# Performance work log

Measured on AMD Instinct MI355X. Metric: run time of the kernel, lower is better.

The kernel has to match this reference:

```python
import jax, jax.numpy as jnp
import numpy as np

N_NODES = 20000
N_EDGES = 320000
MUL = 64            # multiplicity of 0e and 1o in hidden/out irreps
NUM_BASIS = 8
INV_SQRT3 = 0.5773502691896258
EPS = 1e-5


def setup_inputs() -> dict:
    key = jax.random.key(0)
    k = jax.random.split(key, 16)
    return {
        "node_hiddens": jax.random.normal(k[0], (N_NODES, 4 * MUL), dtype=jnp.float32),
        "edge_attr": jax.random.uniform(k[1], (N_EDGES, NUM_BASIS), dtype=jnp.float32),
        "edge_sh": jax.random.normal(k[2], (N_EDGES, 4), dtype=jnp.float32),
        "w1_s": jax.random.normal(k[3], (MUL, MUL), dtype=jnp.float32),
        "w1_v": jax.random.normal(k[4], (MUL, MUL), dtype=jnp.float32),
        "wsc_s": jax.random.normal(k[5], (MUL, MUL), dtype=jnp.float32),
        "wsc_v": jax.random.normal(k[6], (MUL, MUL), dtype=jnp.float32),
        "w2_s": jax.random.normal(k[7], (2 * MUL, MUL), dtype=jnp.float32),
        "w2_v": jax.random.normal(k[8], (2 * MUL, MUL), dtype=jnp.float32),
        "fc_w1": jax.random.normal(k[9], (NUM_BASIS, 64), dtype=jnp.float32),
        "fc_w2": jax.random.normal(k[10], (64, 64), dtype=jnp.float32),
        "fc_w3": jax.random.normal(k[11], (64, 4 * MUL), dtype=jnp.float32),
        "g_s": jnp.ones((MUL,), dtype=jnp.float32),
        "g_v": jnp.ones((MUL,), dtype=jnp.float32),
        "edge_index": jax.random.randint(k[12], (2, N_EDGES), 0, N_NODES),
    }


def reference(node_hiddens, edge_attr, edge_sh, w1_s, w1_v, wsc_s, wsc_v,
              w2_s, w2_v, fc_w1, fc_w2, fc_w3, g_s, g_v, edge_index):
    N = node_hiddens.shape[0]
    # e3nn layout: [N, 64x0e | 64x1o] with mul-major vectors
    xs = node_hiddens[:, :MUL]                        # [N, 64]
    xv = node_hiddens[:, MUL:].reshape(N, MUL, 3)     # [N, 64, 3]

    # edge MLP (FullyConnectedNet([8,64,64,256], silu)) -> per-edge TP weights
    h = jax.nn.silu(edge_attr @ fc_w1 * (1.0 / np.sqrt(float(NUM_BASIS))))
    h = jax.nn.silu(h @ fc_w2 * (1.0 / np.sqrt(64.0)))
    w = h @ fc_w3 * (1.0 / np.sqrt(64.0))             # [E, 4*MUL]
    wA, wB, wC, wD = jnp.split(w, 4, axis=1)          # one 64-vec per uvu path

    inv = 1.0 / np.sqrt(float(MUL))
    # self-connection Linear(hidden -> out)
    sc_s = xs @ wsc_s * inv
    sc_v = jnp.einsum('nud,uv->nvd', xv, wsc_v) * inv
    # linear_1 Linear(hidden -> hidden)
    ys = xs @ w1_s * inv
    yv = jnp.einsum('nud,uv->nvd', xv, w1_v) * inv

    src = edge_index[0]
    dst = edge_index[1]
    es = ys[dst]                                      # [E, 64] gather
    ev = yv[dst]                                      # [E, 64, 3]
    sh0 = edge_sh[:, :1]                              # [E, 1]
    sh1 = edge_sh[:, 1:]                              # [E, 3]

    # weighted uvu Clebsch-Gordan tensor product -> irreps_mid (sorted order)
    m0a = wA * es * sh0                                          # 0e x 0e -> 0e
    m0b = wD * jnp.einsum('eud,ed->eu', ev, sh1) * INV_SQRT3     # 1o x 1o -> 0e
    m1a = wB[:, :, None] * es[:, :, None] * sh1[:, None, :]      # 0e x 1o -> 1o
    m1b = wC[:, :, None] * ev * sh0[:, :, None]                  # 1o x 0e -> 1o
    mid_s = jnp.concatenate([m0a, m0b], axis=1)       # [E, 128]
    mid_v = jnp.concatenate([m1a, m1b], axis=1)       # [E, 128, 3]

    # scatter-sum to source nodes + 1/sqrt(degree) normalization
    ns = jax.ops.segment_sum(mid_s, src, num_segments=N)
    nv = jax.ops.segment_sum(mid_v, src, num_segments=N)
    deg = jax.ops.segment_sum(jnp.ones((src.shape[0],), node_hiddens.dtype), src, num_segments=N)
    dn = jax.lax.rsqrt(jnp.maximum(deg, 1.0))
    ns = ns * dn[:, None]
    nv = nv * dn[:, None, None]

    # linear_2 Linear(128x0e+128x1o -> 64x0e+64x1o) + self connection
    inv2 = 1.0 / np.sqrt(2.0 * MUL)
    os_ = ns @ w2_s * inv2 + sc_s
    ov = jnp.einsum('nud,uv->nvd', nv, w2_v) * inv2 + sc_v

    # equivariant RMS layer norm per irrep type (centering=False)
    os_ = os_ * jax.lax.rsqrt(jnp.mean(os_ * os_, axis=1, keepdims=True) + EPS) * g_s
    rms_v = jax.lax.rsqrt(jnp.mean(ov * ov, axis=(1, 2))[:, None, None] + EPS)
    ov = ov * rms_v * g_v[None, :, None]

    return jnp.concatenate([os_, ov.reshape(N, 3 * MUL)], axis=1)
```

## Files before the change

### kernel.cpp

```cpp
#include <hip/hip_runtime.h>
#include <math.h>

#define N_NODES 20000
#define N_EDGES 320000
#define N_TILES 1250
#define PACK_BLOCKS 32
#define HIST_BLOCKS ((N_EDGES + 255) / 256)
#define SCAT_BLOCKS ((N_EDGES + 255) / 256)
#define K1_BLOCKS ((N_TILES + 3) / 4)

typedef __attribute__((ext_vector_type(8))) short bf16x8;
typedef __attribute__((ext_vector_type(4))) float f32x4;
typedef __attribute__((ext_vector_type(2))) unsigned u32x2;
typedef __attribute__((ext_vector_type(4))) unsigned u32x4;

__device__ __forceinline__ float silu_f(float x) {
    return x / (1.0f + __expf(-x));
}
__device__ __forceinline__ short f2bf(float x) {
    union { float f; unsigned u; } v; v.f = x;
    unsigned r = (v.u + 0x7FFFu + ((v.u >> 16) & 1u)) >> 16;
    return (short)r;
}
__device__ __forceinline__ float blo(unsigned u) { return __uint_as_float(u << 16); }
__device__ __forceinline__ float bhi(unsigned u) { return __uint_as_float(u & 0xFFFF0000u); }
__device__ __forceinline__ unsigned cvt_pk(float lo, float hi) {
    unsigned r;
    asm("v_cvt_pk_bf16_f32 %0, %1, %2" : "=v"(r) : "v"(lo), "v"(hi));
    return r;
}
#define MFMA16(a, b, c) __builtin_amdgcn_mfma_f32_16x16x32_bf16((a), (b), (c), 0, 0, 0)

__global__ __launch_bounds__(256) void kp_hist(
    const int* __restrict__ eidx, int* __restrict__ cnt,
    const float* __restrict__ fcw1, const float* __restrict__ fcw2,
    const float* __restrict__ fcw3,
    const float* __restrict__ w1s, const float* __restrict__ wscs,
    const float* __restrict__ w1v, const float* __restrict__ wscv,
    const float* __restrict__ w2s, const float* __restrict__ w2v,
    short* __restrict__ w1A, short* __restrict__ w2A, short* __restrict__ w3A,
    short* __restrict__ wp1, short* __restrict__ wp2)
{
    if (blockIdx.x >= PACK_BLOCKS) {
        const int e = (blockIdx.x - PACK_BLOCKS) * 256 + threadIdx.x;
        if (e < N_EDGES) atomicAdd(&cnt[eidx[e]], 1);
        return;
    }
    const int tid = blockIdx.x * 256 + threadIdx.x;
    const int nthr = PACK_BLOCKS * 256;
    for (int i = tid; i < 4*64*8; i += nthr) {
        const int j = i & 7, lane = (i >> 3) & 63, t = i >> 9;
        const int k = (lane >> 4) * 8 + j, row = t*16 + (lane & 15);
        w1A[i] = (k < 8) ? f2bf(fcw1[k*64 + row]) : (short)0;
    }
    for (int i = tid; i < 8*64*8; i += nthr) {
        const int j = i & 7, lane = (i >> 3) & 63, kk = (i >> 9) & 1, t = i >> 10;
        const int k = kk*32 + (lane >> 4)*8 + j, row = t*16 + (lane & 15);
        w2A[i] = f2bf(fcw2[k*64 + row]);
    }
    for (int i = tid; i < 32*64*8; i += nthr) {
        const int j = i & 7, lane = (i >> 3) & 63, kk = (i >> 9) & 1, Tp = i >> 10;
        const int c = Tp >> 2, q = Tp & 3;
        const int k = kk*32 + (lane >> 4)*8 + j;
        const int ch = (q*4 + c)*16 + (lane & 15);
        const float s = (ch >= 192) ? 0.5773502691896258f : 1.0f;
        w3A[i] = f2bf(fcw3[(size_t)k*256 + ch] * s);
    }
    for (int i = tid; i < 4096; i += nthr) {
        const int j = i & 7, lane = (i >> 3) & 63, kk = (i >> 9) & 1, vt = i >> 10;
        const int row = vt*16 + (lane & 15), k = kk*32 + (lane >> 4)*8 + j;
        wp1[i]         = f2bf(w1s [k*64 + row]);
        wp1[4096 + i]  = f2bf(wscs[k*64 + row]);
        wp1[8192 + i]  = f2bf(w1v [k*64 + row]);
        wp1[12288 + i] = f2bf(wscv[k*64 + row]);
    }
    for (int i = tid; i < 8192; i += nthr) {
        const int j = i & 7, lane = (i >> 3) & 63, kk = (i >> 9) & 3, vt = i >> 11;
        const int row = vt*16 + (lane & 15), k = kk*32 + (lane >> 4)*8 + j;
        const int r = (k & 1)*64 + (k >> 1);
        wp2[i]        = f2bf(w2s[r*64 + row]);
        wp2[8192 + i] = f2bf(w2v[r*64 + row]);
    }
}

__global__ __launch_bounds__(1024) void s_scan(int* __restrict__ cnt,
                                               int* __restrict__ start) {
    const int tid = threadIdx.x;
    const int base = tid * 20;
    int vals[20];
    int sum = 0;
    #pragma unroll
    for (int j = 0; j < 20; ++j) {
        const int i = base + j;
        const int v = (i < N_NODES) ? cnt[i] : 0;
        vals[j] = sum;
        sum += v;
    }
    const int lane = tid & 63, wv = tid >> 6;
    int x = sum;
    #pragma unroll
    for (int off = 1; off < 64; off <<= 1) {
        const int t = __shfl_up(x, off);
        if (lane >= off) x += t;
    }
    __shared__ int wtot[16];
    if (lane == 63) wtot[wv] = x;
    __syncthreads();
    int wpref = 0;
    for (int k = 0; k < wv; ++k) wpref += wtot[k];
    const int excl = wpref + x - sum;
    #pragma unroll
    for (int j = 0; j < 20; ++j) {
        const int i = base + j;
        if (i < N_NODES) {
            const int s = excl + vals[j];
            start[i] = s;
            cnt[i] = s;
        }
    }
    if (tid == 1023) start[N_NODES] = wpref + x;
}

__global__ __launch_bounds__(256) void scat_k1(
    const int* __restrict__ eidx, int* __restrict__ cursor,
    int* __restrict__ perm, int* __restrict__ dst_perm,
    const float* __restrict__ nh, const short* __restrict__ wp1,
    short* __restrict__ ydata, short* __restrict__ scpack)
{
    if (blockIdx.x < SCAT_BLOCKS) {
        const int e = blockIdx.x * 256 + threadIdx.x;
        if (e < N_EDGES) {
            const int src = eidx[e];
            const int pos = atomicAdd(&cursor[src], 1);
            perm[pos] = e;
            dst_perm[pos] = eidx[N_EDGES + e];
        }
        return;
    }
    const int lane = threadIdx.x & 63;
    const int tile = (blockIdx.x - SCAT_BLOCKS) * 4 + (threadIdx.x >> 6);
    if (tile >= N_TILES) return;
    const int l15 = lane & 15, lhi = lane >> 4;
    const int n = tile*16 + l15;
    const float* row = nh + (size_t)n * 256;
    const f32x4 zz = {0.f, 0.f, 0.f, 0.f};
    f32x4 acc[8][4];
    #pragma unroll
    for (int c = 0; c < 8; ++c)
        #pragma unroll
        for (int vt = 0; vt < 4; ++vt) acc[c][vt] = zz;

    #pragma unroll
    for (int kk = 0; kk < 2; ++kk) {
        const int k0 = kk*32 + lhi*8;
        const float4 s0 = *(const float4*)(row + k0);
        const float4 s1 = *(const float4*)(row + k0 + 4);
        float4 vv[6];
        #pragma unroll
        for (int q = 0; q < 6; ++q) vv[q] = *(const float4*)(row + 64 + 3*k0 + q*4);
        const float* vf = (const float*)vv;
        union { u32x4 u; bf16x8 v; } bs, b0, b1, b2;
        bs.u[0] = cvt_pk(s0.x, s0.y); bs.u[1] = cvt_pk(s0.z, s0.w);
        bs.u[2] = cvt_pk(s1.x, s1.y); bs.u[3] = cvt_pk(s1.z, s1.w);
        #pragma unroll
        for (int q = 0; q < 4; ++q) {
            b0.u[q] = cvt_pk(vf[6*q + 0], vf[6*q + 3]);
            b1.u[q] = cvt_pk(vf[6*q + 1], vf[6*q + 4]);
            b2.u[q] = cvt_pk(vf[6*q + 2], vf[6*q + 5]);
        }
        #pragma unroll
        for (int vt = 0; vt < 4; ++vt) {
            const int fo = ((vt*2 + kk)*64 + lane)*8;
            const bf16x8 a_ys = *(const bf16x8*)&wp1[fo];
            const bf16x8 a_ss = *(const bf16x8*)&wp1[4096 + fo];
            const bf16x8 a_yv = *(const bf16x8*)&wp1[8192 + fo];
            const bf16x8 a_sv = *(const bf16x8*)&wp1[12288 + fo];
            acc[0][vt] = MFMA16(a_ys, bs.v, acc[0][vt]);
            acc[1][vt] = MFMA16(a_ss, bs.v, acc[1][vt]);
            acc[2][vt] = MFMA16(a_yv, b0.v, acc[2][vt]);
            acc[3][vt] = MFMA16(a_yv, b1.v, acc[3][vt]);
            acc[4][vt] = MFMA16(a_yv, b2.v, acc[4][vt]);
            acc[5][vt] = MFMA16(a_sv, b0.v, acc[5][vt]);
            acc[6][vt] = MFMA16(a_sv, b1.v, acc[6][vt]);
            acc[7][vt] = MFMA16(a_sv, b2.v, acc[7][vt]);
        }
    }
    #pragma unroll
    for (int vt = 0; vt < 4; ++vt)
        #pragma unroll
        for (int r = 0; r < 4; ++r) {
            const int v = vt*16 + lhi*4 + r;
            u32x2 yo, so;
            yo[0] = cvt_pk(acc[0][vt][r]*0.125f, acc[2][vt][r]*0.125f);
            yo[1] = cvt_pk(acc[3][vt][r]*0.125f, acc[4][vt][r]*0.125f);
            so[0] = cvt_pk(acc[1][vt][r]*0.125f, acc[5][vt][r]*0.125f);
            so[1] = cvt_pk(acc[6][vt][r]*0.125f, acc[7][vt][r]*0.125f);
            *(u32x2*)&ydata [((size_t)n*64 + v)*4] = yo;
            *(u32x2*)&scpack[((size_t)n*64 + v)*4] = so;
        }
}

__global__ __launch_bounds__(256) void k_mlp(
    const float* __restrict__ ea, const int* __restrict__ perm,
    const short* __restrict__ w1A, const short* __restrict__ w2A,
    const short* __restrict__ w3A, short* __restrict__ wq)
{
    __shared__ short hb1[4][1024];
    __shared__ short hb2[4][1024];
    const int lane = threadIdx.x & 63, w = threadIdx.x >> 6;
    const int l15 = lane & 15, lhi = lane >> 4;
    const int wbase = (blockIdx.x * 4 + w) * 32;
    short* h1b = hb1[w];
    short* h2b = hb2[w];
    const int swz = (l15 & 7) << 4;
    const f32x4 zz = {0.f, 0.f, 0.f, 0.f};

    bf16x8 a1[4], a2[4][2];
    #pragma unroll
    for (int t = 0; t < 4; ++t)
        a1[t] = *(const bf16x8*)&w1A[(t*64 + lane)*8];
    #pragma unroll
    for (int t = 0; t < 4; ++t)
        #pragma unroll
        for (int kk = 0; kk < 2; ++kk)
            a2[t][kk] = *(const bf16x8*)&w2A[((t*2 + kk)*64 + lane)*8];

    bf16x8 bh2[2][2];
    #pragma unroll
    for (int sb = 0; sb < 2; ++sb) {
        bf16x8 bea = {0,0,0,0,0,0,0,0};
        if (lhi == 0) {
            const int e = perm[wbase + sb*16 + l15];
            const float4 p0 = *(const float4*)(ea + (size_t)e*8);
            const float4 p1 = *(const float4*)(ea + (size_t)e*8 + 4);
            union { u32x4 u; bf16x8 v; } tu;
            tu.u[0] = cvt_pk(p0.x, p0.y);
            tu.u[1] = cvt_pk(p0.z, p0.w);
            tu.u[2] = cvt_pk(p1.x, p1.y);
            tu.u[3] = cvt_pk(p1.z, p1.w);
            bea = tu.v;
        }
        f32x4 d1[4];
        #pragma unroll
        for (int t = 0; t < 4; ++t)
            d1[t] = MFMA16(a1[t], bea, zz);
        #pragma unroll
        for (int t = 0; t < 4; ++t) {
            const float s0 = silu_f(d1[t][0] * 0.35355339059327373f);
            const float s1 = silu_f(d1[t][1] * 0.35355339059327373f);
            const float s2 = silu_f(d1[t][2] * 0.35355339059327373f);
            const float s3 = silu_f(d1[t][3] * 0.35355339059327373f);
            u32x2 pk; pk[0] = cvt_pk(s0, s1); pk[1] = cvt_pk(s2, s3);
            const int byt = (l15*128 + t*32 + lhi*8) ^ swz;
            *(u32x2*)((char*)h1b + byt) = pk;
        }
        bf16x8 bh1[2];
        #pragma unroll
        for (int kk = 0; kk < 2; ++kk)
            bh1[kk] = *(const bf16x8*)((const char*)h1b + ((l15*128 + kk*64 + lhi*16) ^ swz));
        f32x4 d2[4];
        #pragma unroll
        for (int t = 0; t < 4; ++t) {
            d2[t] = MFMA16(a2[t][0], bh1[0], zz);
            d2[t] = MFMA16(a2[t][1], bh1[1], d2[t]);
        }
        #pragma unroll
        for (int t = 0; t < 4; ++t) {
            const float s0 = silu_f(d2[t][0] * 0.125f) * 0.125f;
            const float s1 = silu_f(d2[t][1] * 0.125f) * 0.125f;
            const float s2 = silu_f(d2[t][2] * 0.125f) * 0.125f;
            const float s3 = silu_f(d2[t][3] * 0.125f) * 0.125f;
            u32x2 pk; pk[0] = cvt_pk(s0, s1); pk[1] = cvt_pk(s2, s3);
            const int byt = (l15*128 + t*32 + lhi*8) ^ swz;
            *(u32x2*)((char*)h2b + byt) = pk;
        }
        #pragma unroll
        for (int kk = 0; kk < 2; ++kk)
            bh2[sb][kk] = *(const bf16x8*)((const char*)h2b + ((l15*128 + kk*64 + lhi*16) ^ swz));
    }

    #pragma unroll
    for (int c = 0; c < 4; ++c) {
        f32x4 dq[4][2];
        #pragma unroll
        for (int q = 0; q < 4; ++q) {
            const int Tp = c*4 + q;
            const bf16x8 a30 = *(const bf16x8*)&w3A[((Tp*2 + 0)*64 + lane)*8];
            const bf16x8 a31 = *(const bf16x8*)&w3A[((Tp*2 + 1)*64 + lane)*8];
            #pragma unroll
            for (int sb = 0; sb < 2; ++sb) {
                f32x4 d = MFMA16(a30, bh2[sb][0], zz);
                dq[q][sb] = MFMA16(a31, bh2[sb][1], d);
            }
        }
        #pragma unroll
        for (int sb = 0; sb < 2; ++sb) {
            const int slot = wbase + sb*16 + l15;
            const int vbase = c*16 + lhi*4;
            u32x4 lo, hi;
            lo[0] = cvt_pk(dq[0][sb][0], dq[1][sb][0]);
            lo[1] = cvt_pk(dq[2][sb][0], dq[3][sb][0]);
            lo[2] = cvt_pk(dq[0][sb][1], dq[1][sb][1]);
            lo[3] = cvt_pk(dq[2][sb][1], dq[3][sb][1]);
            hi[0] = cvt_pk(dq[0][sb][2], dq[1][sb][2]);
            hi[1] = cvt_pk(dq[2][sb][2], dq[3][sb][2]);
            hi[2] = cvt_pk(dq[0][sb][3], dq[1][sb][3]);
            hi[3] = cvt_pk(dq[2][sb][3], dq[3][sb][3]);
            short* base = &wq[((size_t)slot*64 + vbase)*4];
            *(u32x4*)(base)     = lo;
            *(u32x4*)(base + 8) = hi;
        }
    }
}

__global__ __launch_bounds__(256) void k2_gather(
    const int* __restrict__ start, const int* __restrict__ perm,
    const int* __restrict__ dst_perm, const float* __restrict__ esh,
    const short* __restrict__ wq, const short* __restrict__ ydata,
    unsigned* __restrict__ ncat32)
{
    const int lane = threadIdx.x & 63;
    const int n = blockIdx.x * 4 + (threadIdx.x >> 6);
    if (n >= N_NODES) return;
    const int s0 = start[n], s1 = start[n + 1];
    float acc0=0.f, acc1=0.f, av0=0.f, av1=0.f, av2=0.f, bv0=0.f, bv1=0.f, bv2=0.f;
    for (int p = s0; p < s1; p += 8) {
        const int m = s1 - p;
        u32x2 wv[8], yd[8];
        float4 sh[8];
        int e[8], d[8];
        #pragma unroll
        for (int j = 0; j < 8; ++j) {
            const int pp = (j < m) ? p + j : s0;
            e[j] = perm[pp];
            d[j] = dst_perm[pp];
            wv[j] = *(const u32x2*)&wq[((size_t)pp*64 + lane)*4];
        }
        #pragma unroll
        for (int j = 0; j < 8; ++j) {
            sh[j] = *(const float4*)(esh + (size_t)e[j]*4);
            yd[j] = *(const u32x2*)&ydata[((size_t)d[j]*64 + lane)*4];
        }
        #pragma unroll
        for (int j = 0; j < 8; ++j) {
            const float g = (j < m) ? 1.f : 0.f;
            const float wa = blo(wv[j][0])*g, wb = bhi(wv[j][0])*g;
            const float wc = blo(wv[j][1])*g, wd = bhi(wv[j][1])*g;
            const float es  = blo(yd[j][0]), ev0 = bhi(yd[j][0]);
            const float ev1 = blo(yd[j][1]), ev2 = bhi(yd[j][1]);
            acc0 += wa * es * sh[j].x;
            acc1 += wd * (ev0*sh[j].y + ev1*sh[j].z + ev2*sh[j].w);
            const float esb = wb * es;
            av0 += esb * sh[j].y; av1 += esb * sh[j].z; av2 += esb * sh[j].w;
            const float c0 = wc * sh[j].x;
            bv0 += c0 * ev0; bv1 += c0 * ev1; bv2 += c0 * ev2;
        }
    }
    unsigned* nrow = ncat32 + (size_t)n * 256;
    nrow[lane]        = cvt_pk(acc0, acc1);
    nrow[64  + lane]  = cvt_pk(av0, bv0);
    nrow[128 + lane]  = cvt_pk(av1, bv1);
    nrow[192 + lane]  = cvt_pk(av2, bv2);
}

__global__ __launch_bounds__(256) void k3_mfma(
    const unsigned* __restrict__ ncat32, const int* __restrict__ start,
    const short* __restrict__ wp2, const short* __restrict__ scpack,
    const float* __restrict__ gs, const float* __restrict__ gv,
    float* __restrict__ out)
{
    const int lane = threadIdx.x & 63;
    const int tile = blockIdx.x * 4 + (threadIdx.x >> 6);
    if (tile >= N_TILES) return;
    const int l15 = lane & 15, lhi = lane >> 4;
    const int n = tile*16 + l15;
    const f32x4 zz = {0.f, 0.f, 0.f, 0.f};
    f32x4 acc[4][4];
    #pragma unroll
    for (int c = 0; c < 4; ++c)
        #pragma unroll
        for (int vt = 0; vt < 4; ++vt) acc[c][vt] = zz;

    const size_t nb = (size_t)n * 256;
    #pragma unroll
    for (int kk = 0; kk < 4; ++kk) {
        const int uo = kk*16 + lhi*4;
        union { u32x4 u; bf16x8 v; } bs, b0, b1, b2;
        bs.u = *(const u32x4*)&ncat32[nb +        uo];
        b0.u = *(const u32x4*)&ncat32[nb +  64 + uo];
        b1.u = *(const u32x4*)&ncat32[nb + 128 + uo];
        b2.u = *(const u32x4*)&ncat32[nb + 192 + uo];
        #pragma unroll
        for (int vt = 0; vt < 4; ++vt) {
            const int fo = ((vt*4 + kk)*64 + lane)*8;
            const bf16x8 a_s = *(const bf16x8*)&wp2[fo];
            const bf16x8 a_v = *(const bf16x8*)&wp2[8192 + fo];
            acc[0][vt] = MFMA16(a_s, bs.v, acc[0][vt]);
            acc[1][vt] = MFMA16(a_v, b0.v, acc[1][vt]);
            acc[2][vt] = MFMA16(a_v, b1.v, acc[2][vt]);
            acc[3][vt] = MFMA16(a_v, b2.v, acc[3][vt]);
        }
    }
    const float degf = (float)(start[n+1] - start[n]);
    const float coef = rsqrtf(fmaxf(degf, 1.0f)) * 0.08838834764831845f;
    float os[4][4], o0[4][4], o1[4][4], o2[4][4];
    float ssq = 0.f, vsq = 0.f;
    #pragma unroll
    for (int vt = 0; vt < 4; ++vt)
        #pragma unroll
        for (int r = 0; r < 4; ++r) {
            const int v = vt*16 + lhi*4 + r;
            const u32x2 sc = *(const u32x2*)&scpack[((size_t)n*64 + v)*4];
            os[vt][r] = acc[0][vt][r]*coef + blo(sc[0]);
            o0[vt][r] = acc[1][vt][r]*coef + bhi(sc[0]);
            o1[vt][r] = acc[2][vt][r]*coef + blo(sc[1]);
            o2[vt][r] = acc[3][vt][r]*coef + bhi(sc[1]);
            ssq += os[vt][r]*os[vt][r];
            vsq += o0[vt][r]*o0[vt][r] + o1[vt][r]*o1[vt][r] + o2[vt][r]*o2[vt][r];
        }
    ssq += __shfl_xor(ssq, 16); ssq += __shfl_xor(ssq, 32);
    vsq += __shfl_xor(vsq, 16); vsq += __shfl_xor(vsq, 32);
    const float rs = rsqrtf(ssq * (1.0f/64.0f) + 1e-5f);
    const float rv = rsqrtf(vsq * (1.0f/192.0f) + 1e-5f);
    float* orow = out + (size_t)n * 256;
    #pragma unroll
    for (int vt = 0; vt < 4; ++vt) {
        const int vb = vt*16 + lhi*4;
        const float4 g4  = *(const float4*)(gs + vb);
        const float4 gv4 = *(const float4*)(gv + vb);
        const float4 so = { os[vt][0]*rs*g4.x, os[vt][1]*rs*g4.y,
                            os[vt][2]*rs*g4.z, os[vt][3]*rs*g4.w };
        *(float4*)(orow + vb) = so;
        const float m0 = rv*gv4.x, m1 = rv*gv4.y, m2 = rv*gv4.z, m3 = rv*gv4.w;
        const float4 w0 = { o0[vt][0]*m0, o1[vt][0]*m0, o2[vt][0]*m0, o0[vt][1]*m1 };
        const float4 w1 = { o1[vt][1]*m1, o2[vt][1]*m1, o0[vt][2]*m2, o1[vt][2]*m2 };
        const float4 w2 = { o2[vt][2]*m2, o0[vt][3]*m3, o1[vt][3]*m3, o2[vt][3]*m3 };
        float* vbase = orow + 64 + vb*3;
        *(float4*)(vbase)     = w0;
        *(float4*)(vbase + 4) = w1;
        *(float4*)(vbase + 8) = w2;
    }
}

extern "C" void kernel_launch(void* const* d_in, const int* in_sizes, int n_in,
                              void* d_out, int out_size, void* d_ws, size_t ws_size,
                              hipStream_t stream) {
    const float* nh   = (const float*)d_in[0];
    const float* ea   = (const float*)d_in[1];
    const float* esh  = (const float*)d_in[2];
    const float* w1s  = (const float*)d_in[3];
    const float* w1v  = (const float*)d_in[4];
    const float* wscs = (const float*)d_in[5];
    const float* wscv = (const float*)d_in[6];
    const float* w2s  = (const float*)d_in[7];
    const float* w2v  = (const float*)d_in[8];
    const float* fcw1 = (const float*)d_in[9];
    const float* fcw2 = (const float*)d_in[10];
    const float* fcw3 = (const float*)d_in[11];
    const float* gs   = (const float*)d_in[12];
    const float* gv   = (const float*)d_in[13];
    const int*   eidx = (const int*)d_in[14];
    float* out = (float*)d_out;

    char* wsb = (char*)d_ws;
    size_t off = 0;
    short* ydata  = (short*)(wsb + off); off += (size_t)N_NODES * 256 * 2;
    short* scpack = (short*)(wsb + off); off += (size_t)N_NODES * 256 * 2;
    unsigned* ncat32 = (unsigned*)(wsb + off); off += (size_t)N_NODES * 256 * 4;
    int* cnt      = (int*)(wsb + off); off += (size_t)N_NODES * 4;
    int* start    = (int*)(wsb + off); off += ((size_t)N_NODES + 1) * 4;
    int* perm     = (int*)(wsb + off); off += (size_t)N_EDGES * 4;
    int* dst_perm = (int*)(wsb + off); off += (size_t)N_EDGES * 4;
    short* w1A = (short*)(wsb + off); off += 2048 * 2;
    short* w2A = (short*)(wsb + off); off += 4096 * 2;
    short* w3A = (short*)(wsb + off); off += 16384 * 2;
    short* wp1 = (short*)(wsb + off); off += 16384 * 2;
    short* wp2 = (short*)(wsb + off); off += 16384 * 2;
    off = (off + 15) & ~(size_t)15;
    short* wq = (short*)(wsb + off);

    hipMemsetAsync(cnt, 0, N_NODES * sizeof(int), stream);

    kp_hist<<<PACK_BLOCKS + HIST_BLOCKS, 256, 0, stream>>>(
        eidx, cnt, fcw1, fcw2, fcw3, w1s, wscs, w1v, wscv, w2s, w2v,
        w1A, w2A, w3A, wp1, wp2);

    s_scan<<<1, 1024, 0, stream>>>(cnt, start);

    scat_k1<<<SCAT_BLOCKS + K1_BLOCKS, 256, 0, stream>>>(
        eidx, cnt, perm, dst_perm, nh, wp1, ydata, scpack);

    k_mlp<<<N_EDGES/128, 256, 0, stream>>>(ea, perm, w1A, w2A, w3A, wq);

    k2_gather<<<(N_NODES + 3)/4, 256, 0, stream>>>(
        start, perm, dst_perm, esh, wq, ydata, ncat32);

    k3_mfma<<<(N_TILES + 3)/4, 256, 0, stream>>>(
        ncat32, start, wp2, scpack, gs, gv, out);
}
```

Before: 202.5 us.

## Split edge MLP in halves and overlap second half with gather of finished nodes

The edge MLP now runs in two halves. The second half is fused into one launch with the gather for nodes whose CSR edge ranges fall entirely in the first half. Nodes whose edges reach into the second half are gathered in a separate kernel afterwards. The aim is to overlap MLP compute with memory-bound gather work and fill idle CUs, at the cost of an extra launch and a wasted block sweep in the rest kernel, where most waves exit early.

```diff
diff --git a/kernel.cpp b/kernel.cpp
--- a/kernel.cpp
+++ b/kernel.cpp
@@ -8,6 +8,9 @@
 #define HIST_BLOCKS ((N_EDGES + 255) / 256)
 #define SCAT_BLOCKS ((N_EDGES + 255) / 256)
 #define K1_BLOCKS ((N_TILES + 3) / 4)
+#define MLP_HALF 1250
+#define HALF_EDGES 160000
+#define K2_BLOCKS ((N_NODES + 3) / 4)
 
 typedef __attribute__((ext_vector_type(8))) short bf16x8;
 typedef __attribute__((ext_vector_type(4))) float f32x4;
@@ -200,18 +203,16 @@
         }
 }
 
-__global__ __launch_bounds__(256) void k_mlp(
+__device__ __forceinline__ void mlp_body(
+    const int blk,
     const float* __restrict__ ea, const int* __restrict__ perm,
     const short* __restrict__ w1A, const short* __restrict__ w2A,
-    const short* __restrict__ w3A, short* __restrict__ wq)
-{
-    __shared__ short hb1[4][1024];
-    __shared__ short hb2[4][1024];
+    const short* __restrict__ w3A, short* __restrict__ wq,
+    short* __restrict__ h1b, short* __restrict__ h2b)
+{
     const int lane = threadIdx.x & 63, w = threadIdx.x >> 6;
     const int l15 = lane & 15, lhi = lane >> 4;
-    const int wbase = (blockIdx.x * 4 + w) * 32;
-    short* h1b = hb1[w];
-    short* h2b = hb2[w];
+    const int wbase = (blk * 4 + w) * 32;
     const int swz = (l15 & 7) << 4;
     const f32x4 zz = {0.f, 0.f, 0.f, 0.f};
 
@@ -313,15 +314,13 @@
     }
 }
 
-__global__ __launch_bounds__(256) void k2_gather(
-    const int* __restrict__ start, const int* __restrict__ perm,
+__device__ __forceinline__ void k2_body(
+    const int n, const int* __restrict__ start, const int* __restrict__ perm,
     const int* __restrict__ dst_perm, const float* __restrict__ esh,
     const short* __restrict__ wq, const short* __restrict__ ydata,
     unsigned* __restrict__ ncat32)
 {
     const int lane = threadIdx.x & 63;
-    const int n = blockIdx.x * 4 + (threadIdx.x >> 6);
-    if (n >= N_NODES) return;
     const int s0 = start[n], s1 = start[n + 1];
     float acc0=0.f, acc1=0.f, av0=0.f, av1=0.f, av2=0.f, bv0=0.f, bv1=0.f, bv2=0.f;
     for (int p = s0; p < s1; p += 8) {
@@ -361,6 +360,50 @@
     nrow[64  + lane]  = cvt_pk(av0, bv0);
     nrow[128 + lane]  = cvt_pk(av1, bv1);
     nrow[192 + lane]  = cvt_pk(av2, bv2);
+}
+
+__global__ __launch_bounds__(256) void k_mlp_a(
+    const float* __restrict__ ea, const int* __restrict__ perm,
+    const short* __restrict__ w1A, const short* __restrict__ w2A,
+    const short* __restrict__ w3A, short* __restrict__ wq)
+{
+    __shared__ short hb1[4][1024];
+    __shared__ short hb2[4][1024];
+    const int w = threadIdx.x >> 6;
+    mlp_body(blockIdx.x, ea, perm, w1A, w2A, w3A, wq, hb1[w], hb2[w]);
+}
+
+__global__ __launch_bounds__(256) void mlp_k2(
+    const float* __restrict__ ea, const int* __restrict__ perm,
+    const short* __restrict__ w1A, const short* __restrict__ w2A,
+    const short* __restrict__ w3A, short* __restrict__ wq,
+    const int* __restrict__ start, const int* __restrict__ dst_perm,
+    const float* __restrict__ esh, const short* __restrict__ ydata,
+    unsigned* __restrict__ ncat32)
+{
+    __shared__ short hb1[4][1024];
+    __shared__ short hb2[4][1024];
+    const int w = threadIdx.x >> 6;
+    if (blockIdx.x < MLP_HALF) {
+        mlp_body(MLP_HALF + blockIdx.x, ea, perm, w1A, w2A, w3A, wq, hb1[w], hb2[w]);
+        return;
+    }
+    const int n = (blockIdx.x - MLP_HALF) * 4 + w;
+    if (n >= N_NODES) return;
+    if (start[n + 1] > HALF_EDGES) return;
+    k2_body(n, start, perm, dst_perm, esh, wq, ydata, ncat32);
+}
+
+__global__ __launch_bounds__(256) void k2_rest(
+    const int* __restrict__ start, const int* __restrict__ perm,
+    const int* __restrict__ dst_perm, const float* __restrict__ esh,
+    const short* __restrict__ wq, const short* __restrict__ ydata,
+    unsigned* __restrict__ ncat32)
+{
+    const int n = blockIdx.x * 4 + (threadIdx.x >> 6);
+    if (n >= N_NODES) return;
+    if (start[n + 1] <= HALF_EDGES) return;
+    k2_body(n, start, perm, dst_perm, esh, wq, ydata, ncat32);
 }
 
 __global__ __launch_bounds__(256) void k3_mfma(
@@ -490,9 +533,12 @@
     scat_k1<<<SCAT_BLOCKS + K1_BLOCKS, 256, 0, stream>>>(
         eidx, cnt, perm, dst_perm, nh, wp1, ydata, scpack);
 
-    k_mlp<<<N_EDGES/128, 256, 0, stream>>>(ea, perm, w1A, w2A, w3A, wq);
-
-    k2_gather<<<(N_NODES + 3)/4, 256, 0, stream>>>(
+    k_mlp_a<<<MLP_HALF, 256, 0, stream>>>(ea, perm, w1A, w2A, w3A, wq);
+
+    mlp_k2<<<MLP_HALF + K2_BLOCKS, 256, 0, stream>>>(
+        ea, perm, w1A, w2A, w3A, wq, start, dst_perm, esh, ydata, ncat32);
+
+    k2_rest<<<K2_BLOCKS, 256, 0, stream>>>(
         start, perm, dst_perm, esh, wq, ydata, ncat32);
 
     k3_mfma<<<(N_TILES + 3)/4, 256, 0, stream>>>(
```

New measurement: 226.6 us. 11.9% more time.
